# Performance work log

Hardware: AMD Instinct MI355X
Metric: run time of the kernel (lower is better)

Reference implementation:

```python
import jax, jax.numpy as jnp
import numpy as np

M, OUT, IN = 16384, 2048, 2048

def setup_inputs() -> dict:
    key = jax.random.key(0)
    k1, k2 = jax.random.split(key)
    x = jax.random.normal(k1, (M, IN), dtype=jnp.float32)
    weight = jax.random.normal(k2, (OUT, IN), dtype=jnp.float32)  # nn.Linear weight [out, in]
    alpha = jnp.ones((1,), dtype=jnp.float32) * 0.5
    return {"x": x, "weight": weight, "alpha": alpha}

def reference(x, weight, alpha):
    # DualRateAlphaFunction forward: binarize weight to sign(w) and scale by learned alpha.
    binary_weight = jnp.sign(weight) * alpha  # [out, in]
    # F.linear(x, binary_weight): x @ binary_weight.T
    return jnp.einsum('mi,oi->mo', x, binary_weight)
```

## Files before the change

### kernel.cpp

```cpp
#include <hip/hip_runtime.h>
#include <stdint.h>
#include <type_traits>

#define M_DIM 16384
#define N_DIM 2048
#define K_DIM 2048

typedef __bf16 bf16_t;
typedef __bf16 bf16x8 __attribute__((ext_vector_type(8)));
typedef __bf16 bf16x4 __attribute__((ext_vector_type(4)));
typedef float f32x4 __attribute__((ext_vector_type(4)));

template <int N> using ic = std::integral_constant<int, N>;

__device__ __forceinline__ void gload_lds16(const void* g, void* l) {
  __builtin_amdgcn_global_load_lds(
      (const __attribute__((address_space(1))) void*)g,
      (__attribute__((address_space(3))) void*)l, 16, 0, 0);
}

template <bool SIGN>
__global__ void cvt_kernel(const float* __restrict__ in, bf16_t* __restrict__ out) {
  long long i = ((long long)blockIdx.x * 256 + threadIdx.x) * 8;
  const float4* p = (const float4*)(in + i);
  float4 v0 = p[0];
  float4 v1 = p[1];
  float f[8] = {v0.x, v0.y, v0.z, v0.w, v1.x, v1.y, v1.z, v1.w};
  bf16x8 r;
#pragma unroll
  for (int j = 0; j < 8; ++j) {
    float v = f[j];
    if (SIGN) v = (v > 0.f) ? 1.f : ((v < 0.f) ? -1.f : 0.f);
    r[j] = (bf16_t)v;
  }
  *(bf16x8*)(out + i) = r;
}

__global__ __launch_bounds__(512, 2) void gemm8p(const bf16_t* __restrict__ A,
                                                 const bf16_t* __restrict__ B,
                                                 const float* __restrict__ alpha_p,
                                                 float* __restrict__ C) {
  extern __shared__ char smem[];

  const int tid = threadIdx.x;
  const int lane = tid & 63;
  const int wid = tid >> 6;
  const int wm = wid >> 2;
  const int wn = wid & 3;

  const int bid = blockIdx.x;
  const int swz = (bid & 7) * 64 + (bid >> 3);
  const int bm = swz >> 3;
  const int bn = swz & 7;

  const int q = lane >> 4;
  const int r15 = lane & 15;

  const int swc = (r15 & 7) << 4;
  int aoff[2], boff[2];
#pragma unroll
  for (int k = 0; k < 2; ++k) {
    int ck = (k * 64 + q * 16) ^ swc;
    aoff[k] = (wm * 128 + r15) * 128 + ck;
    boff[k] = 32768 + (wn * 64 + r15) * 128 + ck;
  }

  const char* asrc[4];
  const char* bsrc[4];
  int adsto[4], bdsto[4];
#pragma unroll
  for (int j = 0; j < 4; ++j) {
    int P = j * 8192 + tid * 16;
    int row = P >> 7;
    int lcol = (P & 127) ^ ((row & 7) << 4);
    asrc[j] = (const char*)A + (size_t)(bm * 256 + row) * (K_DIM * 2) + lcol;
    bsrc[j] = (const char*)B + (size_t)(bn * 256 + row) * (K_DIM * 2) + lcol;
    adsto[j] = j * 8192 + wid * 1024;
    bdsto[j] = 32768 + j * 8192 + wid * 1024;
  }

  f32x4 acc[8][4];
#pragma unroll
  for (int mt = 0; mt < 8; ++mt)
#pragma unroll
    for (int nt = 0; nt < 4; ++nt) acc[mt][nt] = (f32x4){0.f, 0.f, 0.f, 0.f};

#pragma unroll
  for (int t = 0; t < 2; ++t) {
#pragma unroll
    for (int j = 0; j < 4; ++j)
      gload_lds16(asrc[j] + t * 128, smem + t * 65536 + adsto[j]);
#pragma unroll
    for (int j = 0; j < 4; ++j)
      gload_lds16(bsrc[j] + t * 128, smem + t * 65536 + bdsto[j]);
  }
  asm volatile("s_waitcnt vmcnt(8)" ::: "memory");
  __builtin_amdgcn_s_barrier();

  auto kstep = [&](auto UC, auto MC) {
    constexpr int U = UC.value;
    constexpr int MODE = MC.value;
    constexpr int TB = U * 65536;
    constexpr int GOFF = (U + 2) * 128;

    bf16x8 a[4][2], bL[2][2], bH[2][2];

#pragma unroll
    for (int mt = 0; mt < 4; ++mt)
#pragma unroll
      for (int k = 0; k < 2; ++k)
        a[mt][k] = *(const bf16x8*)(smem + TB + aoff[k] + mt * 2048);
#pragma unroll
    for (int nt = 0; nt < 2; ++nt)
#pragma unroll
      for (int k = 0; k < 2; ++k)
        bL[nt][k] = *(const bf16x8*)(smem + TB + boff[k] + nt * 2048);
    __builtin_amdgcn_s_barrier();
    asm volatile("s_waitcnt lgkmcnt(0)" ::: "memory");
    __builtin_amdgcn_s_setprio(1);
#pragma unroll
    for (int k = 0; k < 2; ++k)
#pragma unroll
      for (int mt = 0; mt < 4; ++mt)
#pragma unroll
        for (int nt = 0; nt < 2; ++nt)
          acc[mt][nt] = __builtin_amdgcn_mfma_f32_16x16x32_bf16(
              a[mt][k], bL[nt][k], acc[mt][nt], 0, 0, 0);
    __builtin_amdgcn_s_setprio(0);
    __builtin_amdgcn_s_barrier();

#pragma unroll
    for (int nt = 0; nt < 2; ++nt)
#pragma unroll
      for (int k = 0; k < 2; ++k)
        bH[nt][k] = *(const bf16x8*)(smem + TB + boff[k] + (2 + nt) * 2048);
    __builtin_amdgcn_s_barrier();
    asm volatile("s_waitcnt lgkmcnt(0)" ::: "memory");
    __builtin_amdgcn_s_setprio(1);
#pragma unroll
    for (int k = 0; k < 2; ++k)
#pragma unroll
      for (int mt = 0; mt < 4; ++mt)
#pragma unroll
        for (int nt = 0; nt < 2; ++nt)
          acc[mt][2 + nt] = __builtin_amdgcn_mfma_f32_16x16x32_bf16(
              a[mt][k], bH[nt][k], acc[mt][2 + nt], 0, 0, 0);
    __builtin_amdgcn_s_setprio(0);
    __builtin_amdgcn_s_barrier();

#pragma unroll
    for (int mt = 0; mt < 4; ++mt)
#pragma unroll
      for (int k = 0; k < 2; ++k)
        a[mt][k] = *(const bf16x8*)(smem + TB + aoff[k] + (4 + mt) * 2048);
    if constexpr (MODE == 0) {
#pragma unroll
      for (int j = 0; j < 4; ++j)
        gload_lds16(bsrc[j] + GOFF, smem + TB + bdsto[j]);
    }
    __builtin_amdgcn_s_barrier();
    asm volatile("s_waitcnt lgkmcnt(0)" ::: "memory");
    __builtin_amdgcn_s_setprio(1);
#pragma unroll
    for (int k = 0; k < 2; ++k)
#pragma unroll
      for (int mt = 0; mt < 4; ++mt)
#pragma unroll
        for (int nt = 0; nt < 2; ++nt)
          acc[4 + mt][2 + nt] = __builtin_amdgcn_mfma_f32_16x16x32_bf16(
              a[mt][k], bH[nt][k], acc[4 + mt][2 + nt], 0, 0, 0);
    __builtin_amdgcn_s_setprio(0);
    __builtin_amdgcn_s_barrier();

    if constexpr (MODE == 0) {
#pragma unroll
      for (int j = 0; j < 4; ++j)
        gload_lds16(asrc[j] + GOFF, smem + TB + adsto[j]);
      asm volatile("s_waitcnt vmcnt(8)" ::: "memory");
    } else if constexpr (MODE == 1) {
      asm volatile("s_waitcnt vmcnt(0)" ::: "memory");
    }
    __builtin_amdgcn_s_barrier();
    __builtin_amdgcn_s_setprio(1);
#pragma unroll
    for (int k = 0; k < 2; ++k)
#pragma unroll
      for (int mt = 0; mt < 4; ++mt)
#pragma unroll
        for (int nt = 0; nt < 2; ++nt)
          acc[4 + mt][nt] = __builtin_amdgcn_mfma_f32_16x16x32_bf16(
              a[mt][k], bL[nt][k], acc[4 + mt][nt], 0, 0, 0);
    __builtin_amdgcn_s_setprio(0);
    __builtin_amdgcn_s_barrier();
  };

#pragma unroll 1
  for (int T = 0; T < 15; ++T) {
    kstep(ic<0>{}, ic<0>{});
    kstep(ic<1>{}, ic<0>{});
#pragma unroll
    for (int j = 0; j < 4; ++j) { asrc[j] += 256; bsrc[j] += 256; }
  }
  kstep(ic<0>{}, ic<1>{});
  kstep(ic<1>{}, ic<2>{});

  const float alpha = alpha_p[0];
  const int rbase = bm * 256 + wm * 128 + q * 4;
  const int cbase = bn * 256 + wn * 64 + r15;
#pragma unroll
  for (int mt = 0; mt < 8; ++mt)
#pragma unroll
    for (int nt = 0; nt < 4; ++nt)
#pragma unroll
      for (int r = 0; r < 4; ++r)
        C[(size_t)(rbase + mt * 16 + r) * N_DIM + cbase + nt * 16] =
            alpha * acc[mt][nt][r];
}

__global__ __launch_bounds__(256) void gemm_fallback(const float* __restrict__ Ap,
                                                     const float* __restrict__ Bp,
                                                     const float* __restrict__ alpha_p,
                                                     float* __restrict__ C) {
  __shared__ bf16_t Asf[128 * 32];
  __shared__ bf16_t Bsf[128 * 32];
  const int tid = threadIdx.x;
  const int lane = tid & 63;
  const int wid = tid >> 6;
  const int wr = wid >> 1;
  const int wc = wid & 1;
  const int cpx = gridDim.x >> 3;
  const int bid = blockIdx.x;
  const int swz = (bid & 7) * cpx + (bid >> 3);
  const int NB = N_DIM / 128;
  const int bm = swz / NB;
  const int bn = swz % NB;
  f32x4 acc[4][4];
#pragma unroll
  for (int m = 0; m < 4; ++m)
#pragma unroll
    for (int n = 0; n < 4; ++n) acc[m][n] = (f32x4){0.f, 0.f, 0.f, 0.f};
  const int r0 = lane & 15;
  const int ko = (lane >> 4) * 8;
  for (int kk = 0; kk < K_DIM; kk += 32) {
    const float* Af = Ap + (size_t)bm * 128 * K_DIM + kk;
    const float* Bf = Bp + (size_t)bn * 128 * K_DIM + kk;
#pragma unroll
    for (int qq = 0; qq < 4; ++qq) {
      int e = qq * 256 + tid;
      int row = e >> 3;
      int kc = (e & 7) << 2;
      float4 v = *(const float4*)(Af + (size_t)row * K_DIM + kc);
      bf16x4 tv;
      tv[0] = (bf16_t)v.x; tv[1] = (bf16_t)v.y; tv[2] = (bf16_t)v.z; tv[3] = (bf16_t)v.w;
      *(bf16x4*)&Asf[e * 4] = tv;
    }
#pragma unroll
    for (int qq = 0; qq < 4; ++qq) {
      int e = qq * 256 + tid;
      int row = e >> 3;
      int kc = (e & 7) << 2;
      float4 v = *(const float4*)(Bf + (size_t)row * K_DIM + kc);
      float s[4] = {v.x, v.y, v.z, v.w};
      bf16x4 tv;
#pragma unroll
      for (int j = 0; j < 4; ++j)
        tv[j] = (bf16_t)((s[j] > 0.f) ? 1.f : ((s[j] < 0.f) ? -1.f : 0.f));
      *(bf16x4*)&Bsf[e * 4] = tv;
    }
    __syncthreads();
    bf16x8 a[4], b[4];
#pragma unroll
    for (int m = 0; m < 4; ++m) a[m] = *(const bf16x8*)&Asf[(wr * 64 + m * 16 + r0) * 32 + ko];
#pragma unroll
    for (int n = 0; n < 4; ++n) b[n] = *(const bf16x8*)&Bsf[(wc * 64 + n * 16 + r0) * 32 + ko];
#pragma unroll
    for (int m = 0; m < 4; ++m)
#pragma unroll
      for (int n = 0; n < 4; ++n)
        acc[m][n] = __builtin_amdgcn_mfma_f32_16x16x32_bf16(a[m], b[n], acc[m][n], 0, 0, 0);
    __syncthreads();
  }
  const float alpha = alpha_p[0];
  const int rowb = bm * 128 + wr * 64 + (lane >> 4) * 4;
  const int colb = bn * 128 + wc * 64 + r0;
#pragma unroll
  for (int m = 0; m < 4; ++m)
#pragma unroll
    for (int n = 0; n < 4; ++n)
#pragma unroll
      for (int r = 0; r < 4; ++r)
        C[(size_t)(rowb + m * 16 + r) * N_DIM + colb + n * 16] = alpha * acc[m][n][r];
}

extern "C" void kernel_launch(void* const* d_in, const int* in_sizes, int n_in,
                              void* d_out, int out_size, void* d_ws, size_t ws_size,
                              hipStream_t stream) {
  const float* x = (const float*)d_in[0];
  const float* w = (const float*)d_in[1];
  const float* alpha = (const float*)d_in[2];
  float* out = (float*)d_out;

  const size_t nx = (size_t)M_DIM * K_DIM;
  const size_t nw = (size_t)N_DIM * K_DIM;
  const size_t need = (nx + nw) * sizeof(bf16_t);

  if (ws_size >= need) {
    bf16_t* xb = (bf16_t*)d_ws;
    bf16_t* wb = xb + nx;
    cvt_kernel<false><<<(int)(nx / 2048), 256, 0, stream>>>(x, xb);
    cvt_kernel<true><<<(int)(nw / 2048), 256, 0, stream>>>(w, wb);
    (void)hipFuncSetAttribute((const void*)gemm8p,
                              hipFuncAttributeMaxDynamicSharedMemorySize, 131072);
    gemm8p<<<512, 512, 131072, stream>>>(xb, wb, alpha, out);
  } else {
    gemm_fallback<<<(M_DIM / 128) * (N_DIM / 128), 256, 0, stream>>>(x, w, alpha, out);
  }
}
```

Baseline: 168.5 us.

## Overlap LDS fragment reads with MFMAs using partial lgkmcnt waits

Restructures the per-k-step schedule from four barrier-separated phases into three. LDS reads for bL, a and bH are issued together and followed by graduated lgkmcnt waits, so MFMA groups can start before all operands arrive. Sched barriers pin the instruction order so the compiler does not undo the interleaving. This aims to hide LDS latency and remove one workgroup barrier per phase, at the cost of more live registers and reliance on exact LDS counter arithmetic.

```diff
diff --git a/kernel.cpp b/kernel.cpp
--- a/kernel.cpp
+++ b/kernel.cpp
@@ -12,6 +12,8 @@
 typedef float f32x4 __attribute__((ext_vector_type(4)));
 
 template <int N> using ic = std::integral_constant<int, N>;
+
+#define SB0() __builtin_amdgcn_sched_barrier(0)
 
 __device__ __forceinline__ void gload_lds16(const void* g, void* l) {
   __builtin_amdgcn_global_load_lds(
@@ -106,65 +108,104 @@
     bf16x8 a[4][2], bL[2][2], bH[2][2];
 
 #pragma unroll
-    for (int mt = 0; mt < 4; ++mt)
+    for (int nt = 0; nt < 2; ++nt)
+#pragma unroll
+      for (int k = 0; k < 2; ++k)
+        bL[nt][k] = *(const bf16x8*)(smem + TB + boff[k] + nt * 2048);
+#pragma unroll
+    for (int mt = 0; mt < 2; ++mt)
 #pragma unroll
       for (int k = 0; k < 2; ++k)
         a[mt][k] = *(const bf16x8*)(smem + TB + aoff[k] + mt * 2048);
-#pragma unroll
-    for (int nt = 0; nt < 2; ++nt)
-#pragma unroll
-      for (int k = 0; k < 2; ++k)
-        bL[nt][k] = *(const bf16x8*)(smem + TB + boff[k] + nt * 2048);
-    __builtin_amdgcn_s_barrier();
-    asm volatile("s_waitcnt lgkmcnt(0)" ::: "memory");
+    SB0();
+#pragma unroll
+    for (int mt = 2; mt < 4; ++mt)
+#pragma unroll
+      for (int k = 0; k < 2; ++k)
+        a[mt][k] = *(const bf16x8*)(smem + TB + aoff[k] + mt * 2048);
+    SB0();
+#pragma unroll
+    for (int k = 0; k < 2; ++k)
+      bH[0][k] = *(const bf16x8*)(smem + TB + boff[k] + 2 * 2048);
+    SB0();
+#pragma unroll
+    for (int k = 0; k < 2; ++k)
+      bH[1][k] = *(const bf16x8*)(smem + TB + boff[k] + 3 * 2048);
+    __builtin_amdgcn_s_barrier();
+    asm volatile("s_waitcnt lgkmcnt(8)" ::: "memory");
+    SB0();
     __builtin_amdgcn_s_setprio(1);
 #pragma unroll
     for (int k = 0; k < 2; ++k)
 #pragma unroll
-      for (int mt = 0; mt < 4; ++mt)
+      for (int mt = 0; mt < 2; ++mt)
 #pragma unroll
         for (int nt = 0; nt < 2; ++nt)
           acc[mt][nt] = __builtin_amdgcn_mfma_f32_16x16x32_bf16(
               a[mt][k], bL[nt][k], acc[mt][nt], 0, 0, 0);
+    asm volatile("s_waitcnt lgkmcnt(4)" ::: "memory");
+    SB0();
+#pragma unroll
+    for (int k = 0; k < 2; ++k)
+#pragma unroll
+      for (int mt = 2; mt < 4; ++mt)
+#pragma unroll
+        for (int nt = 0; nt < 2; ++nt)
+          acc[mt][nt] = __builtin_amdgcn_mfma_f32_16x16x32_bf16(
+              a[mt][k], bL[nt][k], acc[mt][nt], 0, 0, 0);
+    asm volatile("s_waitcnt lgkmcnt(2)" ::: "memory");
+    SB0();
+#pragma unroll
+    for (int k = 0; k < 2; ++k)
+#pragma unroll
+      for (int mt = 0; mt < 4; ++mt)
+        acc[mt][2] = __builtin_amdgcn_mfma_f32_16x16x32_bf16(
+            a[mt][k], bH[0][k], acc[mt][2], 0, 0, 0);
+    asm volatile("s_waitcnt lgkmcnt(0)" ::: "memory");
+    SB0();
+#pragma unroll
+    for (int k = 0; k < 2; ++k)
+#pragma unroll
+      for (int mt = 0; mt < 4; ++mt)
+        acc[mt][3] = __builtin_amdgcn_mfma_f32_16x16x32_bf16(
+            a[mt][k], bH[1][k], acc[mt][3], 0, 0, 0);
     __builtin_amdgcn_s_setprio(0);
     __builtin_amdgcn_s_barrier();
 
-#pragma unroll
-    for (int nt = 0; nt < 2; ++nt)
-#pragma unroll
-      for (int k = 0; k < 2; ++k)
-        bH[nt][k] = *(const bf16x8*)(smem + TB + boff[k] + (2 + nt) * 2048);
-    __builtin_amdgcn_s_barrier();
-    asm volatile("s_waitcnt lgkmcnt(0)" ::: "memory");
-    __builtin_amdgcn_s_setprio(1);
-#pragma unroll
-    for (int k = 0; k < 2; ++k)
-#pragma unroll
-      for (int mt = 0; mt < 4; ++mt)
-#pragma unroll
-        for (int nt = 0; nt < 2; ++nt)
-          acc[mt][2 + nt] = __builtin_amdgcn_mfma_f32_16x16x32_bf16(
-              a[mt][k], bH[nt][k], acc[mt][2 + nt], 0, 0, 0);
-    __builtin_amdgcn_s_setprio(0);
-    __builtin_amdgcn_s_barrier();
-
-#pragma unroll
-    for (int mt = 0; mt < 4; ++mt)
-#pragma unroll
-      for (int k = 0; k < 2; ++k)
-        a[mt][k] = *(const bf16x8*)(smem + TB + aoff[k] + (4 + mt) * 2048);
     if constexpr (MODE == 0) {
 #pragma unroll
       for (int j = 0; j < 4; ++j)
         gload_lds16(bsrc[j] + GOFF, smem + TB + bdsto[j]);
     }
-    __builtin_amdgcn_s_barrier();
+#pragma unroll
+    for (int mt = 0; mt < 2; ++mt)
+#pragma unroll
+      for (int k = 0; k < 2; ++k)
+        a[mt][k] = *(const bf16x8*)(smem + TB + aoff[k] + (4 + mt) * 2048);
+    SB0();
+#pragma unroll
+    for (int mt = 2; mt < 4; ++mt)
+#pragma unroll
+      for (int k = 0; k < 2; ++k)
+        a[mt][k] = *(const bf16x8*)(smem + TB + aoff[k] + (4 + mt) * 2048);
+    __builtin_amdgcn_s_barrier();
+    asm volatile("s_waitcnt lgkmcnt(4)" ::: "memory");
+    SB0();
+    __builtin_amdgcn_s_setprio(1);
+#pragma unroll
+    for (int k = 0; k < 2; ++k)
+#pragma unroll
+      for (int mt = 0; mt < 2; ++mt)
+#pragma unroll
+        for (int nt = 0; nt < 2; ++nt)
+          acc[4 + mt][2 + nt] = __builtin_amdgcn_mfma_f32_16x16x32_bf16(
+              a[mt][k], bH[nt][k], acc[4 + mt][2 + nt], 0, 0, 0);
     asm volatile("s_waitcnt lgkmcnt(0)" ::: "memory");
-    __builtin_amdgcn_s_setprio(1);
-#pragma unroll
-    for (int k = 0; k < 2; ++k)
-#pragma unroll
-      for (int mt = 0; mt < 4; ++mt)
+    SB0();
+#pragma unroll
+    for (int k = 0; k < 2; ++k)
+#pragma unroll
+      for (int mt = 2; mt < 4; ++mt)
 #pragma unroll
         for (int nt = 0; nt < 2; ++nt)
           acc[4 + mt][2 + nt] = __builtin_amdgcn_mfma_f32_16x16x32_bf16(
@@ -181,6 +222,7 @@
       asm volatile("s_waitcnt vmcnt(0)" ::: "memory");
     }
     __builtin_amdgcn_s_barrier();
+    SB0();
     __builtin_amdgcn_s_setprio(1);
 #pragma unroll
     for (int k = 0; k < 2; ++k)
```

New measurement: 168.6 us. About the same (+0.1%).

## Restructure GEMM k-step to one barrier per stage with cross-stage A prefetch

Applied to the files above, without the earlier changes.

Each k-step of the bf16 MFMA GEMM drops from eight workgroup barriers to one. All B fragments and the upper A fragments are loaded up front, three MFMA quadrants run back to back, and the global-to-LDS refill is issued after a single vmcnt(0) wait and barrier. The lower A fragments for the next buffer are prefetched into registers before the last MFMA quadrant, so LDS reads overlap compute across stages. Sched barriers pin the instruction order. This cuts synchronisation overhead but raises register pressure, and waiting for vmcnt(0) each step leaves less global-load latency hidden behind compute.

```diff
diff --git a/kernel.cpp b/kernel.cpp
--- a/kernel.cpp
+++ b/kernel.cpp
@@ -12,6 +12,8 @@
 typedef float f32x4 __attribute__((ext_vector_type(4)));
 
 template <int N> using ic = std::integral_constant<int, N>;
+
+#define SB0() __builtin_amdgcn_sched_barrier(0)
 
 __device__ __forceinline__ void gload_lds16(const void* g, void* l) {
   __builtin_amdgcn_global_load_lds(
@@ -36,7 +38,7 @@
   *(bf16x8*)(out + i) = r;
 }
 
-__global__ __launch_bounds__(512, 2) void gemm8p(const bf16_t* __restrict__ A,
+__global__ __launch_bounds__(512, 2) void gemm1b(const bf16_t* __restrict__ A,
                                                  const bf16_t* __restrict__ B,
                                                  const float* __restrict__ alpha_p,
                                                  float* __restrict__ C) {
@@ -85,6 +87,8 @@
 #pragma unroll
     for (int nt = 0; nt < 4; ++nt) acc[mt][nt] = (f32x4){0.f, 0.f, 0.f, 0.f};
 
+  bf16x8 aLo[4][2];
+
 #pragma unroll
   for (int t = 0; t < 2; ++t) {
 #pragma unroll
@@ -95,28 +99,40 @@
       gload_lds16(bsrc[j] + t * 128, smem + t * 65536 + bdsto[j]);
   }
   asm volatile("s_waitcnt vmcnt(8)" ::: "memory");
+  SB0();
   __builtin_amdgcn_s_barrier();
+  SB0();
+#pragma unroll
+  for (int mt = 0; mt < 4; ++mt)
+#pragma unroll
+    for (int k = 0; k < 2; ++k)
+      aLo[mt][k] = *(const bf16x8*)(smem + aoff[k] + mt * 2048);
 
   auto kstep = [&](auto UC, auto MC) {
     constexpr int U = UC.value;
     constexpr int MODE = MC.value;
     constexpr int TB = U * 65536;
+    constexpr int NTB = ((U + 1) & 1) * 65536;
     constexpr int GOFF = (U + 2) * 128;
 
-    bf16x8 a[4][2], bL[2][2], bH[2][2];
-
-#pragma unroll
-    for (int mt = 0; mt < 4; ++mt)
-#pragma unroll
-      for (int k = 0; k < 2; ++k)
-        a[mt][k] = *(const bf16x8*)(smem + TB + aoff[k] + mt * 2048);
+    bf16x8 bL[2][2], bH[2][2], aH[4][2];
+
 #pragma unroll
     for (int nt = 0; nt < 2; ++nt)
 #pragma unroll
       for (int k = 0; k < 2; ++k)
         bL[nt][k] = *(const bf16x8*)(smem + TB + boff[k] + nt * 2048);
-    __builtin_amdgcn_s_barrier();
-    asm volatile("s_waitcnt lgkmcnt(0)" ::: "memory");
+#pragma unroll
+    for (int nt = 0; nt < 2; ++nt)
+#pragma unroll
+      for (int k = 0; k < 2; ++k)
+        bH[nt][k] = *(const bf16x8*)(smem + TB + boff[k] + (2 + nt) * 2048);
+#pragma unroll
+    for (int mt = 0; mt < 4; ++mt)
+#pragma unroll
+      for (int k = 0; k < 2; ++k)
+        aH[mt][k] = *(const bf16x8*)(smem + TB + aoff[k] + (4 + mt) * 2048);
+    SB0();
     __builtin_amdgcn_s_setprio(1);
 #pragma unroll
     for (int k = 0; k < 2; ++k)
@@ -125,18 +141,7 @@
 #pragma unroll
         for (int nt = 0; nt < 2; ++nt)
           acc[mt][nt] = __builtin_amdgcn_mfma_f32_16x16x32_bf16(
-              a[mt][k], bL[nt][k], acc[mt][nt], 0, 0, 0);
-    __builtin_amdgcn_s_setprio(0);
-    __builtin_amdgcn_s_barrier();
-
-#pragma unroll
-    for (int nt = 0; nt < 2; ++nt)
-#pragma unroll
-      for (int k = 0; k < 2; ++k)
-        bH[nt][k] = *(const bf16x8*)(smem + TB + boff[k] + (2 + nt) * 2048);
-    __builtin_amdgcn_s_barrier();
-    asm volatile("s_waitcnt lgkmcnt(0)" ::: "memory");
-    __builtin_amdgcn_s_setprio(1);
+              aLo[mt][k], bL[nt][k], acc[mt][nt], 0, 0, 0);
 #pragma unroll
     for (int k = 0; k < 2; ++k)
 #pragma unroll
@@ -144,43 +149,38 @@
 #pragma unroll
         for (int nt = 0; nt < 2; ++nt)
           acc[mt][2 + nt] = __builtin_amdgcn_mfma_f32_16x16x32_bf16(
-              a[mt][k], bH[nt][k], acc[mt][2 + nt], 0, 0, 0);
+              aLo[mt][k], bH[nt][k], acc[mt][2 + nt], 0, 0, 0);
+#pragma unroll
+    for (int k = 0; k < 2; ++k)
+#pragma unroll
+      for (int mt = 0; mt < 4; ++mt)
+#pragma unroll
+        for (int nt = 0; nt < 2; ++nt)
+          acc[4 + mt][2 + nt] = __builtin_amdgcn_mfma_f32_16x16x32_bf16(
+              aH[mt][k], bH[nt][k], acc[4 + mt][2 + nt], 0, 0, 0);
     __builtin_amdgcn_s_setprio(0);
+    SB0();
+    asm volatile("s_waitcnt vmcnt(0)" ::: "memory");
+    SB0();
     __builtin_amdgcn_s_barrier();
-
-#pragma unroll
-    for (int mt = 0; mt < 4; ++mt)
-#pragma unroll
-      for (int k = 0; k < 2; ++k)
-        a[mt][k] = *(const bf16x8*)(smem + TB + aoff[k] + (4 + mt) * 2048);
+    SB0();
+
     if constexpr (MODE == 0) {
 #pragma unroll
       for (int j = 0; j < 4; ++j)
         gload_lds16(bsrc[j] + GOFF, smem + TB + bdsto[j]);
-    }
-    __builtin_amdgcn_s_barrier();
-    asm volatile("s_waitcnt lgkmcnt(0)" ::: "memory");
-    __builtin_amdgcn_s_setprio(1);
-#pragma unroll
-    for (int k = 0; k < 2; ++k)
-#pragma unroll
-      for (int mt = 0; mt < 4; ++mt)
-#pragma unroll
-        for (int nt = 0; nt < 2; ++nt)
-          acc[4 + mt][2 + nt] = __builtin_amdgcn_mfma_f32_16x16x32_bf16(
-              a[mt][k], bH[nt][k], acc[4 + mt][2 + nt], 0, 0, 0);
-    __builtin_amdgcn_s_setprio(0);
-    __builtin_amdgcn_s_barrier();
-
-    if constexpr (MODE == 0) {
 #pragma unroll
       for (int j = 0; j < 4; ++j)
         gload_lds16(asrc[j] + GOFF, smem + TB + adsto[j]);
-      asm volatile("s_waitcnt vmcnt(8)" ::: "memory");
-    } else if constexpr (MODE == 1) {
-      asm volatile("s_waitcnt vmcnt(0)" ::: "memory");
     }
-    __builtin_amdgcn_s_barrier();
+    if constexpr (MODE != 2) {
+#pragma unroll
+      for (int mt = 0; mt < 4; ++mt)
+#pragma unroll
+        for (int k = 0; k < 2; ++k)
+          aLo[mt][k] = *(const bf16x8*)(smem + NTB + aoff[k] + mt * 2048);
+    }
+    SB0();
     __builtin_amdgcn_s_setprio(1);
 #pragma unroll
     for (int k = 0; k < 2; ++k)
@@ -189,9 +189,9 @@
 #pragma unroll
         for (int nt = 0; nt < 2; ++nt)
           acc[4 + mt][nt] = __builtin_amdgcn_mfma_f32_16x16x32_bf16(
-              a[mt][k], bL[nt][k], acc[4 + mt][nt], 0, 0, 0);
+              aH[mt][k], bL[nt][k], acc[4 + mt][nt], 0, 0, 0);
     __builtin_amdgcn_s_setprio(0);
-    __builtin_amdgcn_s_barrier();
+    SB0();
   };
 
 #pragma unroll 1
@@ -309,9 +309,9 @@
     bf16_t* wb = xb + nx;
     cvt_kernel<false><<<(int)(nx / 2048), 256, 0, stream>>>(x, xb);
     cvt_kernel<true><<<(int)(nw / 2048), 256, 0, stream>>>(w, wb);
-    (void)hipFuncSetAttribute((const void*)gemm8p,
+    (void)hipFuncSetAttribute((const void*)gemm1b,
                               hipFuncAttributeMaxDynamicSharedMemorySize, 131072);
-    gemm8p<<<512, 512, 131072, stream>>>(xb, wb, alpha, out);
+    gemm1b<<<512, 512, 131072, stream>>>(xb, wb, alpha, out);
   } else {
     gemm_fallback<<<(M_DIM / 128) * (N_DIM / 128), 256, 0, stream>>>(x, w, alpha, out);
   }
```

Result: slower. 287.9 us (+70.9%).

## Load B fragments directly from global into registers and triple-buffer A in LDS

Applied to the files above, without the earlier changes.

The GEMM no longer stages the binarized weight tile through LDS. Each wave loads its B fragments straight from global memory into double-buffered registers, while A goes through a three-slot LDS ring with fewer barriers per k-step. This is meant to cut LDS traffic and synchronisation overhead and to lower LDS usage to 96KB. In exchange, B reads become uncoalesced 16-byte per-lane global loads duplicated across waves, and register pressure rises.

```diff
diff --git a/kernel.cpp b/kernel.cpp
--- a/kernel.cpp
+++ b/kernel.cpp
@@ -36,10 +36,10 @@
   *(bf16x8*)(out + i) = r;
 }
 
-__global__ __launch_bounds__(512, 2) void gemm8p(const bf16_t* __restrict__ A,
-                                                 const bf16_t* __restrict__ B,
-                                                 const float* __restrict__ alpha_p,
-                                                 float* __restrict__ C) {
+__global__ __launch_bounds__(512, 2) void gemm_bg(const bf16_t* __restrict__ A,
+                                                  const bf16_t* __restrict__ B,
+                                                  const float* __restrict__ alpha_p,
+                                                  float* __restrict__ C) {
   extern __shared__ char smem[];
 
   const int tid = threadIdx.x;
@@ -57,27 +57,26 @@
   const int r15 = lane & 15;
 
   const int swc = (r15 & 7) << 4;
-  int aoff[2], boff[2];
-#pragma unroll
-  for (int k = 0; k < 2; ++k) {
-    int ck = (k * 64 + q * 16) ^ swc;
-    aoff[k] = (wm * 128 + r15) * 128 + ck;
-    boff[k] = 32768 + (wn * 64 + r15) * 128 + ck;
-  }
-
-  const char* asrc[4];
-  const char* bsrc[4];
-  int adsto[4], bdsto[4];
-#pragma unroll
-  for (int j = 0; j < 4; ++j) {
-    int P = j * 8192 + tid * 16;
+  int aoff[2];
+#pragma unroll
+  for (int k = 0; k < 2; ++k)
+    aoff[k] = (wm * 128 + r15) * 128 + ((k * 64 + q * 16) ^ swc);
+
+  const char* asrc0;
+  {
+    int P = tid * 16;
     int row = P >> 7;
     int lcol = (P & 127) ^ ((row & 7) << 4);
-    asrc[j] = (const char*)A + (size_t)(bm * 256 + row) * (K_DIM * 2) + lcol;
-    bsrc[j] = (const char*)B + (size_t)(bn * 256 + row) * (K_DIM * 2) + lcol;
-    adsto[j] = j * 8192 + wid * 1024;
-    bdsto[j] = 32768 + j * 8192 + wid * 1024;
-  }
+    asrc0 = (const char*)A + (size_t)(bm * 256 + row) * (K_DIM * 2) + lcol;
+  }
+  const int dsto = wid * 1024;
+
+  const char* baddr[4];
+#pragma unroll
+  for (int nt = 0; nt < 4; ++nt)
+    baddr[nt] = (const char*)B +
+                (size_t)(bn * 256 + wn * 64 + nt * 16 + r15) * (K_DIM * 2) +
+                q * 16;
 
   f32x4 acc[8][4];
 #pragma unroll
@@ -85,121 +84,94 @@
 #pragma unroll
     for (int nt = 0; nt < 4; ++nt) acc[mt][nt] = (f32x4){0.f, 0.f, 0.f, 0.f};
 
-#pragma unroll
-  for (int t = 0; t < 2; ++t) {
+  bf16x8 bfr[2][4][2];
+
+#pragma unroll
+  for (int t = 0; t < 2; ++t)
 #pragma unroll
     for (int j = 0; j < 4; ++j)
-      gload_lds16(asrc[j] + t * 128, smem + t * 65536 + adsto[j]);
-#pragma unroll
-    for (int j = 0; j < 4; ++j)
-      gload_lds16(bsrc[j] + t * 128, smem + t * 65536 + bdsto[j]);
-  }
-  asm volatile("s_waitcnt vmcnt(8)" ::: "memory");
-  __builtin_amdgcn_s_barrier();
+      gload_lds16(asrc0 + (size_t)j * 262144 + t * 128,
+                  smem + t * 32768 + j * 8192 + dsto);
+#pragma unroll
+  for (int nt = 0; nt < 4; ++nt)
+#pragma unroll
+    for (int k2 = 0; k2 < 2; ++k2)
+      bfr[0][nt][k2] = *(const bf16x8*)(baddr[nt] + k2 * 64);
+  asm volatile("s_waitcnt vmcnt(12)" ::: "memory");
 
   auto kstep = [&](auto UC, auto MC) {
     constexpr int U = UC.value;
     constexpr int MODE = MC.value;
-    constexpr int TB = U * 65536;
+    constexpr int SLOT = (U % 3) * 32768;
+    constexpr int PSLOT = ((U + 2) % 3) * 32768;
     constexpr int GOFF = (U + 2) * 128;
-
-    bf16x8 a[4][2], bL[2][2], bH[2][2];
-
+    constexpr int BOFF = (U + 1) * 128;
+    constexpr int PAR = U & 1;
+
+    __builtin_amdgcn_s_barrier();
+
+    if constexpr (MODE != 2) {
+#pragma unroll
+      for (int nt = 0; nt < 4; ++nt)
+#pragma unroll
+        for (int k2 = 0; k2 < 2; ++k2)
+          bfr[PAR ^ 1][nt][k2] =
+              *(const bf16x8*)(baddr[nt] + BOFF + k2 * 64);
+    }
+    if constexpr (MODE == 0) {
+#pragma unroll
+      for (int j = 0; j < 4; ++j)
+        gload_lds16(asrc0 + (size_t)j * 262144 + GOFF,
+                    smem + PSLOT + j * 8192 + dsto);
+    }
+    if constexpr (MODE == 0) {
+      asm volatile("s_waitcnt vmcnt(12)" ::: "memory");
+    } else if constexpr (MODE == 1) {
+      asm volatile("s_waitcnt vmcnt(8)" ::: "memory");
+    } else {
+      asm volatile("s_waitcnt vmcnt(0)" ::: "memory");
+    }
+
+    bf16x8 a[4][2];
 #pragma unroll
     for (int mt = 0; mt < 4; ++mt)
 #pragma unroll
       for (int k = 0; k < 2; ++k)
-        a[mt][k] = *(const bf16x8*)(smem + TB + aoff[k] + mt * 2048);
-#pragma unroll
-    for (int nt = 0; nt < 2; ++nt)
+        a[mt][k] = *(const bf16x8*)(smem + SLOT + aoff[k] + mt * 2048);
+#pragma unroll
+    for (int k = 0; k < 2; ++k)
+#pragma unroll
+      for (int mt = 0; mt < 4; ++mt)
+#pragma unroll
+        for (int nt = 0; nt < 4; ++nt)
+          acc[mt][nt] = __builtin_amdgcn_mfma_f32_16x16x32_bf16(
+              a[mt][k], bfr[PAR][nt][k], acc[mt][nt], 0, 0, 0);
+#pragma unroll
+    for (int mt = 0; mt < 4; ++mt)
 #pragma unroll
       for (int k = 0; k < 2; ++k)
-        bL[nt][k] = *(const bf16x8*)(smem + TB + boff[k] + nt * 2048);
-    __builtin_amdgcn_s_barrier();
-    asm volatile("s_waitcnt lgkmcnt(0)" ::: "memory");
-    __builtin_amdgcn_s_setprio(1);
+        a[mt][k] = *(const bf16x8*)(smem + SLOT + aoff[k] + (4 + mt) * 2048);
 #pragma unroll
     for (int k = 0; k < 2; ++k)
 #pragma unroll
       for (int mt = 0; mt < 4; ++mt)
 #pragma unroll
-        for (int nt = 0; nt < 2; ++nt)
-          acc[mt][nt] = __builtin_amdgcn_mfma_f32_16x16x32_bf16(
-              a[mt][k], bL[nt][k], acc[mt][nt], 0, 0, 0);
-    __builtin_amdgcn_s_setprio(0);
-    __builtin_amdgcn_s_barrier();
-
-#pragma unroll
-    for (int nt = 0; nt < 2; ++nt)
-#pragma unroll
-      for (int k = 0; k < 2; ++k)
-        bH[nt][k] = *(const bf16x8*)(smem + TB + boff[k] + (2 + nt) * 2048);
-    __builtin_amdgcn_s_barrier();
-    asm volatile("s_waitcnt lgkmcnt(0)" ::: "memory");
-    __builtin_amdgcn_s_setprio(1);
-#pragma unroll
-    for (int k = 0; k < 2; ++k)
-#pragma unroll
-      for (int mt = 0; mt < 4; ++mt)
-#pragma unroll
-        for (int nt = 0; nt < 2; ++nt)
-          acc[mt][2 + nt] = __builtin_amdgcn_mfma_f32_16x16x32_bf16(
-              a[mt][k], bH[nt][k], acc[mt][2 + nt], 0, 0, 0);
-    __builtin_amdgcn_s_setprio(0);
-    __builtin_amdgcn_s_barrier();
-
-#pragma unroll
-    for (int mt = 0; mt < 4; ++mt)
-#pragma unroll
-      for (int k = 0; k < 2; ++k)
-        a[mt][k] = *(const bf16x8*)(smem + TB + aoff[k] + (4 + mt) * 2048);
-    if constexpr (MODE == 0) {
-#pragma unroll
-      for (int j = 0; j < 4; ++j)
-        gload_lds16(bsrc[j] + GOFF, smem + TB + bdsto[j]);
-    }
-    __builtin_amdgcn_s_barrier();
-    asm volatile("s_waitcnt lgkmcnt(0)" ::: "memory");
-    __builtin_amdgcn_s_setprio(1);
-#pragma unroll
-    for (int k = 0; k < 2; ++k)
-#pragma unroll
-      for (int mt = 0; mt < 4; ++mt)
-#pragma unroll
-        for (int nt = 0; nt < 2; ++nt)
-          acc[4 + mt][2 + nt] = __builtin_amdgcn_mfma_f32_16x16x32_bf16(
-              a[mt][k], bH[nt][k], acc[4 + mt][2 + nt], 0, 0, 0);
-    __builtin_amdgcn_s_setprio(0);
-    __builtin_amdgcn_s_barrier();
-
-    if constexpr (MODE == 0) {
-#pragma unroll
-      for (int j = 0; j < 4; ++j)
-        gload_lds16(asrc[j] + GOFF, smem + TB + adsto[j]);
-      asm volatile("s_waitcnt vmcnt(8)" ::: "memory");
-    } else if constexpr (MODE == 1) {
-      asm volatile("s_waitcnt vmcnt(0)" ::: "memory");
-    }
-    __builtin_amdgcn_s_barrier();
-    __builtin_amdgcn_s_setprio(1);
-#pragma unroll
-    for (int k = 0; k < 2; ++k)
-#pragma unroll
-      for (int mt = 0; mt < 4; ++mt)
-#pragma unroll
-        for (int nt = 0; nt < 2; ++nt)
+        for (int nt = 0; nt < 4; ++nt)
           acc[4 + mt][nt] = __builtin_amdgcn_mfma_f32_16x16x32_bf16(
-              a[mt][k], bL[nt][k], acc[4 + mt][nt], 0, 0, 0);
-    __builtin_amdgcn_s_setprio(0);
-    __builtin_amdgcn_s_barrier();
+              a[mt][k], bfr[PAR][nt][k], acc[4 + mt][nt], 0, 0, 0);
   };
 
 #pragma unroll 1
-  for (int T = 0; T < 15; ++T) {
+  for (int W = 0; W < 5; ++W) {
     kstep(ic<0>{}, ic<0>{});
     kstep(ic<1>{}, ic<0>{});
-#pragma unroll
-    for (int j = 0; j < 4; ++j) { asrc[j] += 256; bsrc[j] += 256; }
+    kstep(ic<2>{}, ic<0>{});
+    kstep(ic<3>{}, ic<0>{});
+    kstep(ic<4>{}, ic<0>{});
+    kstep(ic<5>{}, ic<0>{});
+    asrc0 += 768;
+#pragma unroll
+    for (int nt = 0; nt < 4; ++nt) baddr[nt] += 768;
   }
   kstep(ic<0>{}, ic<1>{});
   kstep(ic<1>{}, ic<2>{});
@@ -309,9 +281,9 @@
     bf16_t* wb = xb + nx;
     cvt_kernel<false><<<(int)(nx / 2048), 256, 0, stream>>>(x, xb);
     cvt_kernel<true><<<(int)(nw / 2048), 256, 0, stream>>>(w, wb);
-    (void)hipFuncSetAttribute((const void*)gemm8p,
-                              hipFuncAttributeMaxDynamicSharedMemorySize, 131072);
-    gemm8p<<<512, 512, 131072, stream>>>(xb, wb, alpha, out);
+    (void)hipFuncSetAttribute((const void*)gemm_bg,
+                              hipFuncAttributeMaxDynamicSharedMemorySize, 98304);
+    gemm_bg<<<512, 512, 98304, stream>>>(xb, wb, alpha, out);
   } else {
     gemm_fallback<<<(M_DIM / 128) * (N_DIM / 128), 256, 0, stream>>>(x, w, alpha, out);
   }
```

After: 221.4 us. 31.4% more time.
